# Kernel tuning notes

Hardware: AMD Instinct MI355X
Metric: run time of the kernel (lower is better)

The kernel has to match this reference:

```python
import jax, jax.numpy as jnp
import numpy as np

N_NODES = 100000
N_EDGES = 1600000  # avg degree 16
D_FEAT = 128


def setup_inputs() -> dict:
    key = jax.random.key(0)
    k1, k2, k3 = jax.random.split(key, 3)
    x = jax.random.normal(k1, (N_NODES, D_FEAT), dtype=jnp.float32)
    edge_index = jax.random.randint(k2, (2, N_EDGES), 0, N_NODES, dtype=jnp.int64)
    edge_values = jax.random.uniform(k3, (N_EDGES,), dtype=jnp.float32)
    return {"x": x, "edge_index": edge_index, "edge_values": edge_values}


def reference(x, edge_index, edge_values):
    # torch_sparse.spmm(indices, values, N, N, x):
    # out[row_e] += values[e] * x[col_e]  for each COO edge e.
    row, col = edge_index[0], edge_index[1]
    msgs = edge_values[:, None] * x[col]              # [E, D] gathered messages
    out = jax.ops.segment_sum(msgs, row, num_segments=x.shape[0])  # [N, D]
    return out
```

## Files before the change

### kernel.cpp

```cpp
#include <hip/hip_runtime.h>
#include <hip/hip_bf16.h>


#define D_FEAT 128
#define CAP 32
#define CAP_S 40
#define OVF_CAP 8192
#define CONV_BLOCKS 1024
#define EPB 2048
#define BIN_SHIFT 9
#define SEG_CAP 9216

typedef float f32x4 __attribute__((ext_vector_type(4)));

static __device__ __forceinline__ unsigned short f2bf(float f) {
    unsigned u = __float_as_uint(f);
    u += 0x7fffu + ((u >> 16) & 1u);
    return (unsigned short)(u >> 16);
}


__global__ __launch_bounds__(256) void conv_part_kernel(
    const float* __restrict__ x, unsigned* __restrict__ xq32,
    float* __restrict__ scales, int N,
    const int* __restrict__ rows, const int* __restrict__ cols,
    const float* __restrict__ w,
    int* __restrict__ binfill,
    unsigned long long* __restrict__ part,
    unsigned long long* __restrict__ ovf,
    int E) {
    __shared__ unsigned long long ldsbuf[EPB];
    __shared__ int hist[256];
    __shared__ int tmp[256];
    __shared__ int boff[256];
    __shared__ int base_s[256];

    int tid = threadIdx.x;

    if (blockIdx.x < CONV_BLOCKS) {
        int grp = tid >> 5;
        int gl  = tid & 31;
        const float4* x4 = reinterpret_cast<const float4*>(x);
        for (int r = blockIdx.x * 8 + grp; r < N; r += CONV_BLOCKS * 8) {
            float4 v = x4[(size_t)r * 32 + gl];
            float m = fmaxf(fmaxf(fabsf(v.x), fabsf(v.y)),
                            fmaxf(fabsf(v.z), fabsf(v.w)));
            m = fmaxf(m, __shfl_xor(m, 1));
            m = fmaxf(m, __shfl_xor(m, 2));
            m = fmaxf(m, __shfl_xor(m, 4));
            m = fmaxf(m, __shfl_xor(m, 8));
            m = fmaxf(m, __shfl_xor(m, 16));
            float rs = (m > 0.f) ? 127.0f / m : 0.f;
            int q0 = __float2int_rn(v.x * rs) + 128;
            int q1 = __float2int_rn(v.y * rs) + 128;
            int q2 = __float2int_rn(v.z * rs) + 128;
            int q3 = __float2int_rn(v.w * rs) + 128;
            q0 = min(max(q0, 0), 255); q1 = min(max(q1, 0), 255);
            q2 = min(max(q2, 0), 255); q3 = min(max(q3, 0), 255);
            unsigned pk = (unsigned)q0 | ((unsigned)q1 << 8)
                        | ((unsigned)q2 << 16) | ((unsigned)q3 << 24);
            __builtin_nontemporal_store(pk, &xq32[(size_t)r * 32 + gl]);
            if (gl == 0) scales[r] = m * (1.0f / 127.0f);
        }
        return;
    }

    int pb = blockIdx.x - CONV_BLOCKS;
    int ebase = pb * EPB;

    hist[tid] = 0;
    __syncthreads();

    unsigned long long e64[8];
    unsigned meta[8];
#pragma unroll 8
    for (int j = 0; j < 8; ++j) {
        int idx = ebase + tid + j * 256;
        if (idx < E) {
            int r = rows[idx];
            int c = cols[idx];
            float wv = w[idx];
            int bin = r >> BIN_SHIFT;
            int rk = atomicAdd(&hist[bin], 1);
            e64[j] = (unsigned long long)(unsigned)r
                   | ((unsigned long long)(unsigned)c << 17)
                   | ((unsigned long long)f2bf(wv) << 34);
            meta[j] = ((unsigned)bin << 13) | (unsigned)rk;
        } else {
            meta[j] = 0xffffffffu;
        }
    }
    __syncthreads();

    int hv = hist[tid];
    tmp[tid] = hv;
    __syncthreads();
    for (int off = 1; off < 256; off <<= 1) {
        int t = (tid >= off) ? tmp[tid - off] : 0;
        __syncthreads();
        tmp[tid] += t;
        __syncthreads();
    }
    boff[tid] = tmp[tid] - hv;
    int total = tmp[255];

    base_s[tid] = atomicAdd(&binfill[tid], hv);
#pragma unroll 8
    for (int j = 0; j < 8; ++j) {
        if (meta[j] != 0xffffffffu) {
            int bin = meta[j] >> 13;
            int rk = meta[j] & 0x1fff;
            ldsbuf[boff[bin] + rk] = e64[j];
        }
    }
    __syncthreads();

    int* ovfcnt = binfill + 256;
    for (int k = tid; k < total; k += 256) {
        unsigned long long e = ldsbuf[k];
        int bin = (int)(e & 0x1ffffu) >> BIN_SHIFT;
        int pos = base_s[bin] + (k - boff[bin]);
        if (pos < SEG_CAP) {
            part[(size_t)bin * SEG_CAP + pos] = e;
        } else {
            int o = atomicAdd(ovfcnt, 1);
            if (o < OVF_CAP) ovf[o] = e;
        }
    }
}


__global__ __launch_bounds__(512) void bucketize_kernel(
    const unsigned long long* __restrict__ part, int* __restrict__ binfill,
    const float* __restrict__ scales,
    unsigned* __restrict__ packed, int* __restrict__ cursor,
    unsigned long long* __restrict__ ovf, int N) {
    __shared__ int cnt[512];
    int b = blockIdx.x;
    int tid = threadIdx.x;
    cnt[tid] = 0;
    __syncthreads();

    int fill = min(binfill[b], SEG_CAP);
    int rbase = b << BIN_SHIFT;
    const unsigned long long* seg = part + (size_t)b * SEG_CAP;
    int* ovfcnt = binfill + 256;

    for (int k = tid; k < fill; k += 512) {
        unsigned long long e = seg[k];
        int r = (int)(e & 0x1ffffu);
        int rk = atomicAdd(&cnt[r - rbase], 1);
        if (rk < CAP) {
            unsigned c = (unsigned)(e >> 17) & 0x1ffffu;
            float wv = __uint_as_float((unsigned)((e >> 34) & 0xffffu) << 16);
            float wf = wv * scales[c];
            packed[(size_t)r * CAP_S + rk] = c | ((unsigned)f2bf(wf) << 17);
        } else {
            int o = atomicAdd(ovfcnt, 1);
            if (o < OVF_CAP) ovf[o] = e;
        }
    }
    __syncthreads();

    int r = rbase + tid;
    if (r < N) {
        int d = min(cnt[tid], CAP);
        int pad = min((d + 7) & ~7, CAP);
        unsigned* pb = packed + (size_t)r * CAP_S;
        for (int k = d; k < pad; ++k) pb[k] = 0u;
        cursor[r] = pad;
    }
}


__global__ __launch_bounds__(256) void spmm_cap_kernel(
    const unsigned* __restrict__ xq32,
    const int* __restrict__ cursor, const unsigned* __restrict__ packed,
    float* __restrict__ out, int N) {
    int wid = (int)((blockIdx.x * 256 + threadIdx.x) >> 6);
    int lane = threadIdx.x & 63;
    int gl = lane & 31;
    bool hi = lane >= 32;
    if (wid >= N) return;

    int deg = cursor[wid];
    float a0 = 0.f, a1 = 0.f, a2 = 0.f, a3 = 0.f, sumw = 0.f;

    if (deg > 0) {
        const unsigned* base = packed + (size_t)wid * CAP_S;
        const unsigned* xl = xq32 + gl;
        uint4 pa = *reinterpret_cast<const uint4*>(base);
        uint4 pb = *reinterpret_cast<const uint4*>(base + 4);
        for (int e = 0; e < deg; e += 8) {
            const unsigned* nb = base + e + 8;
            uint4 qa = *reinterpret_cast<const uint4*>(nb);
            uint4 qb = *reinterpret_cast<const uint4*>(nb + 4);
            unsigned e0 = hi ? pa.y : pa.x;
            unsigned e1 = hi ? pa.w : pa.z;
            unsigned e2 = hi ? pb.y : pb.x;
            unsigned e3 = hi ? pb.w : pb.z;
            unsigned u0 = xl[(e0 & 0x1ffffu) << 5];
            unsigned u1 = xl[(e1 & 0x1ffffu) << 5];
            unsigned u2 = xl[(e2 & 0x1ffffu) << 5];
            unsigned u3 = xl[(e3 & 0x1ffffu) << 5];
            float w0 = __uint_as_float((e0 >> 17) << 16);
            float w1 = __uint_as_float((e1 >> 17) << 16);
            float w2 = __uint_as_float((e2 >> 17) << 16);
            float w3 = __uint_as_float((e3 >> 17) << 16);
            a0 += w0 * (float)(u0 & 0xffu);
            a1 += w0 * (float)((u0 >> 8) & 0xffu);
            a2 += w0 * (float)((u0 >> 16) & 0xffu);
            a3 += w0 * (float)(u0 >> 24);
            a0 += w1 * (float)(u1 & 0xffu);
            a1 += w1 * (float)((u1 >> 8) & 0xffu);
            a2 += w1 * (float)((u1 >> 16) & 0xffu);
            a3 += w1 * (float)(u1 >> 24);
            a0 += w2 * (float)(u2 & 0xffu);
            a1 += w2 * (float)((u2 >> 8) & 0xffu);
            a2 += w2 * (float)((u2 >> 16) & 0xffu);
            a3 += w2 * (float)(u2 >> 24);
            a0 += w3 * (float)(u3 & 0xffu);
            a1 += w3 * (float)((u3 >> 8) & 0xffu);
            a2 += w3 * (float)((u3 >> 16) & 0xffu);
            a3 += w3 * (float)(u3 >> 24);
            sumw += w0 + w1 + w2 + w3;
            pa = qa; pb = qb;
        }
    }
    a0 -= 128.0f * sumw; a1 -= 128.0f * sumw;
    a2 -= 128.0f * sumw; a3 -= 128.0f * sumw;
    a0 += __shfl_xor(a0, 32);
    a1 += __shfl_xor(a1, 32);
    a2 += __shfl_xor(a2, 32);
    a3 += __shfl_xor(a3, 32);
    if (!hi) {
        f32x4 o; o.x = a0; o.y = a1; o.z = a2; o.w = a3;
        __builtin_nontemporal_store(
            o, reinterpret_cast<f32x4*>(out) + (size_t)wid * 32 + gl);
    }
}


__global__ __launch_bounds__(256) void cleanup_kernel(
    const float* __restrict__ x, const unsigned long long* __restrict__ ovf,
    const int* __restrict__ binfill, float* __restrict__ out) {
    int t = blockIdx.x * 256 + threadIdx.x;
    int i = t >> 5;
    int part_ = t & 31;
    int cnt = min(binfill[256], OVF_CAP);
    if (i >= cnt) return;
    unsigned long long e = ovf[i];
    int r = (int)(e & 0x1ffffu);
    int c = (int)((e >> 17) & 0x1ffffu);
    float wv = __uint_as_float((unsigned)((e >> 34) & 0xffffu) << 16);
    const float4* xr = reinterpret_cast<const float4*>(x + (size_t)c * D_FEAT);
    float4 v = xr[part_];
    float* o = out + (size_t)r * D_FEAT + part_ * 4;
    unsafeAtomicAdd(o + 0, v.x * wv);
    unsafeAtomicAdd(o + 1, v.y * wv);
    unsafeAtomicAdd(o + 2, v.z * wv);
    unsafeAtomicAdd(o + 3, v.w * wv);
}


__global__ __launch_bounds__(256) void spmm_scatter_kernel(
    const float* __restrict__ x, const int* __restrict__ edge_index,
    const float* __restrict__ edge_values, float* __restrict__ out, int E) {
    long long t = (long long)blockIdx.x * blockDim.x + threadIdx.x;
    int e = (int)(t >> 5);
    int part = (int)(t & 31);
    if (e >= E) return;
    int row = edge_index[e];
    int col = edge_index[E + e];
    float w = edge_values[e];
    const float4* xrow = reinterpret_cast<const float4*>(x + (size_t)col * D_FEAT);
    float4 v = xrow[part];
    float* o = out + (size_t)row * D_FEAT + part * 4;
    unsafeAtomicAdd(o + 0, v.x * w);
    unsafeAtomicAdd(o + 1, v.y * w);
    unsafeAtomicAdd(o + 2, v.z * w);
    unsafeAtomicAdd(o + 3, v.w * w);
}


extern "C" void kernel_launch(void* const* d_in, const int* in_sizes, int n_in,
                              void* d_out, int out_size, void* d_ws, size_t ws_size,
                              hipStream_t stream) {
    const float* x           = (const float*)d_in[0];
    const int*   edge_index  = (const int*)d_in[1];
    const float* edge_values = (const float*)d_in[2];
    float*       out         = (float*)d_out;

    int E = in_sizes[2];
    int N = out_size / D_FEAT;
    const int* rows = edge_index;
    const int* cols = edge_index + E;
    int nbins = (N + (1 << BIN_SHIFT) - 1) >> BIN_SHIFT;

    size_t off = 0;
    int* cursor  = (int*)((char*)d_ws + off); off += (size_t)N * sizeof(int);
    int* binfill = (int*)((char*)d_ws + off); off += 257 * sizeof(int);
    off = (off + 127) & ~(size_t)127;
    float* scales = (float*)((char*)d_ws + off); off += (size_t)N * sizeof(float);
    off = (off + 127) & ~(size_t)127;
    unsigned long long* ovf = (unsigned long long*)((char*)d_ws + off);
    off += (size_t)OVF_CAP * sizeof(unsigned long long);
    unsigned long long* part = (unsigned long long*)((char*)d_ws + off);
    off += (size_t)nbins * SEG_CAP * sizeof(unsigned long long);
    off = (off + 127) & ~(size_t)127;
    unsigned* packed = (unsigned*)((char*)d_ws + off);
    off += (size_t)N * CAP_S * sizeof(unsigned);
    off = (off + 127) & ~(size_t)127;
    unsigned* xq32 = (unsigned*)((char*)d_ws + off);
    off += (size_t)N * 32 * sizeof(unsigned);

    if (off <= ws_size && N <= (1 << 17) && nbins <= 256) {
        int pbl = (E + EPB - 1) / EPB;
        int gbl = (int)(((long long)N * 64 + 255) / 256);
        hipMemsetAsync(binfill, 0, 257 * sizeof(int), stream);
        conv_part_kernel<<<CONV_BLOCKS + pbl, 256, 0, stream>>>(
            x, xq32, scales, N, rows, cols, edge_values, binfill, part, ovf, E);
        bucketize_kernel<<<nbins, 512, 0, stream>>>(
            part, binfill, scales, packed, cursor, ovf, N);
        spmm_cap_kernel<<<gbl, 256, 0, stream>>>(
            xq32, cursor, packed, out, N);
        cleanup_kernel<<<(OVF_CAP * 32) / 256, 256, 0, stream>>>(
            x, ovf, binfill, out);
        return;
    }

    hipMemsetAsync(d_out, 0, (size_t)out_size * sizeof(float), stream);
    long long total_threads = (long long)E * 32;
    long long grid = (total_threads + 255) / 256;
    spmm_scatter_kernel<<<(dim3)(unsigned)grid, 256, 0, stream>>>(
        x, edge_index, edge_values, out, E);
}
```

Before: 107.4 us.

## Process two rows per wavefront in spmm and use wave-shuffle scan for bins

The spmm kernel now assigns two output rows to each 64-lane wavefront and interleaves their gathers, which halves the wave count and doubles the memory-level parallelism per wave. Each row's weight sum is reduced across the wave once before it is subtracted. The block prefix scan in the partition kernel is replaced with a shuffle-based wave scan plus a small cross-wave add, removing many __syncthreads. Padding now zeroes each row to CAP so the shared loop bound max(degA,degB) reads zeros for the shorter row, which costs extra stores and wasted iterations when the two degrees differ.

```diff
diff --git a/kernel.cpp b/kernel.cpp
--- a/kernel.cpp
+++ b/kernel.cpp
@@ -31,9 +31,9 @@
     int E) {
     __shared__ unsigned long long ldsbuf[EPB];
     __shared__ int hist[256];
-    __shared__ int tmp[256];
     __shared__ int boff[256];
     __shared__ int base_s[256];
+    __shared__ int wsum[4];
 
     int tid = threadIdx.x;
 
@@ -93,16 +93,21 @@
     __syncthreads();
 
     int hv = hist[tid];
-    tmp[tid] = hv;
-    __syncthreads();
-    for (int off = 1; off < 256; off <<= 1) {
-        int t = (tid >= off) ? tmp[tid - off] : 0;
-        __syncthreads();
-        tmp[tid] += t;
-        __syncthreads();
-    }
-    boff[tid] = tmp[tid] - hv;
-    int total = tmp[255];
+    int s = hv;
+#pragma unroll
+    for (int d = 1; d < 64; d <<= 1) {
+        int t = __shfl_up(s, d);
+        if ((tid & 63) >= d) s += t;
+    }
+    if ((tid & 63) == 63) wsum[tid >> 6] = s;
+    __syncthreads();
+    int wv_ = tid >> 6;
+    int add = 0;
+#pragma unroll
+    for (int k = 0; k < 4; ++k) add += (k < wv_) ? wsum[k] : 0;
+    boff[tid] = s - hv + add;
+    int total = wsum[0] + wsum[1] + wsum[2] + wsum[3];
+    __syncthreads();
 
     base_s[tid] = atomicAdd(&binfill[tid], hv);
 #pragma unroll 8
@@ -165,9 +170,9 @@
     int r = rbase + tid;
     if (r < N) {
         int d = min(cnt[tid], CAP);
-        int pad = min((d + 7) & ~7, CAP);
+        int pad = (d + 7) & ~7;
         unsigned* pb = packed + (size_t)r * CAP_S;
-        for (int k = d; k < pad; ++k) pb[k] = 0u;
+        for (int k = d; k < CAP; ++k) pb[k] = 0u;
         cursor[r] = pad;
     }
 }
@@ -177,66 +182,116 @@
     const unsigned* __restrict__ xq32,
     const int* __restrict__ cursor, const unsigned* __restrict__ packed,
     float* __restrict__ out, int N) {
-    int wid = (int)((blockIdx.x * 256 + threadIdx.x) >> 6);
+    int gw = (int)((blockIdx.x * 256 + threadIdx.x) >> 6);
+    int rA = gw * 2;
+    if (rA >= N) return;
+    int rB = rA + 1;
+    bool hasB = rB < N;
     int lane = threadIdx.x & 63;
     int gl = lane & 31;
     bool hi = lane >= 32;
-    if (wid >= N) return;
-
-    int deg = cursor[wid];
-    float a0 = 0.f, a1 = 0.f, a2 = 0.f, a3 = 0.f, sumw = 0.f;
+
+    int degA = cursor[rA];
+    int degB = hasB ? cursor[rB] : 0;
+    int deg = max(degA, degB);
+
+    float a0 = 0.f, a1 = 0.f, a2 = 0.f, a3 = 0.f, swA = 0.f;
+    float b0 = 0.f, b1 = 0.f, b2 = 0.f, b3 = 0.f, swB = 0.f;
 
     if (deg > 0) {
-        const unsigned* base = packed + (size_t)wid * CAP_S;
+        const unsigned* baseA = packed + (size_t)rA * CAP_S;
+        const unsigned* baseB = packed + (size_t)(hasB ? rB : rA) * CAP_S;
         const unsigned* xl = xq32 + gl;
-        uint4 pa = *reinterpret_cast<const uint4*>(base);
-        uint4 pb = *reinterpret_cast<const uint4*>(base + 4);
+        uint4 paA = *reinterpret_cast<const uint4*>(baseA);
+        uint4 pbA = *reinterpret_cast<const uint4*>(baseA + 4);
+        uint4 paB = *reinterpret_cast<const uint4*>(baseB);
+        uint4 pbB = *reinterpret_cast<const uint4*>(baseB + 4);
         for (int e = 0; e < deg; e += 8) {
-            const unsigned* nb = base + e + 8;
-            uint4 qa = *reinterpret_cast<const uint4*>(nb);
-            uint4 qb = *reinterpret_cast<const uint4*>(nb + 4);
-            unsigned e0 = hi ? pa.y : pa.x;
-            unsigned e1 = hi ? pa.w : pa.z;
-            unsigned e2 = hi ? pb.y : pb.x;
-            unsigned e3 = hi ? pb.w : pb.z;
-            unsigned u0 = xl[(e0 & 0x1ffffu) << 5];
-            unsigned u1 = xl[(e1 & 0x1ffffu) << 5];
-            unsigned u2 = xl[(e2 & 0x1ffffu) << 5];
-            unsigned u3 = xl[(e3 & 0x1ffffu) << 5];
-            float w0 = __uint_as_float((e0 >> 17) << 16);
-            float w1 = __uint_as_float((e1 >> 17) << 16);
-            float w2 = __uint_as_float((e2 >> 17) << 16);
-            float w3 = __uint_as_float((e3 >> 17) << 16);
-            a0 += w0 * (float)(u0 & 0xffu);
-            a1 += w0 * (float)((u0 >> 8) & 0xffu);
-            a2 += w0 * (float)((u0 >> 16) & 0xffu);
-            a3 += w0 * (float)(u0 >> 24);
-            a0 += w1 * (float)(u1 & 0xffu);
-            a1 += w1 * (float)((u1 >> 8) & 0xffu);
-            a2 += w1 * (float)((u1 >> 16) & 0xffu);
-            a3 += w1 * (float)(u1 >> 24);
-            a0 += w2 * (float)(u2 & 0xffu);
-            a1 += w2 * (float)((u2 >> 8) & 0xffu);
-            a2 += w2 * (float)((u2 >> 16) & 0xffu);
-            a3 += w2 * (float)(u2 >> 24);
-            a0 += w3 * (float)(u3 & 0xffu);
-            a1 += w3 * (float)((u3 >> 8) & 0xffu);
-            a2 += w3 * (float)((u3 >> 16) & 0xffu);
-            a3 += w3 * (float)(u3 >> 24);
-            sumw += w0 + w1 + w2 + w3;
-            pa = qa; pb = qb;
-        }
-    }
-    a0 -= 128.0f * sumw; a1 -= 128.0f * sumw;
-    a2 -= 128.0f * sumw; a3 -= 128.0f * sumw;
-    a0 += __shfl_xor(a0, 32);
-    a1 += __shfl_xor(a1, 32);
-    a2 += __shfl_xor(a2, 32);
-    a3 += __shfl_xor(a3, 32);
+            const unsigned* nA = baseA + e + 8;
+            const unsigned* nB = baseB + e + 8;
+            uint4 qaA = *reinterpret_cast<const uint4*>(nA);
+            uint4 qbA = *reinterpret_cast<const uint4*>(nA + 4);
+            uint4 qaB = *reinterpret_cast<const uint4*>(nB);
+            uint4 qbB = *reinterpret_cast<const uint4*>(nB + 4);
+            unsigned eA0 = hi ? paA.y : paA.x;
+            unsigned eA1 = hi ? paA.w : paA.z;
+            unsigned eA2 = hi ? pbA.y : pbA.x;
+            unsigned eA3 = hi ? pbA.w : pbA.z;
+            unsigned eB0 = hi ? paB.y : paB.x;
+            unsigned eB1 = hi ? paB.w : paB.z;
+            unsigned eB2 = hi ? pbB.y : pbB.x;
+            unsigned eB3 = hi ? pbB.w : pbB.z;
+            unsigned uA0 = xl[(eA0 & 0x1ffffu) << 5];
+            unsigned uA1 = xl[(eA1 & 0x1ffffu) << 5];
+            unsigned uA2 = xl[(eA2 & 0x1ffffu) << 5];
+            unsigned uA3 = xl[(eA3 & 0x1ffffu) << 5];
+            unsigned uB0 = xl[(eB0 & 0x1ffffu) << 5];
+            unsigned uB1 = xl[(eB1 & 0x1ffffu) << 5];
+            unsigned uB2 = xl[(eB2 & 0x1ffffu) << 5];
+            unsigned uB3 = xl[(eB3 & 0x1ffffu) << 5];
+            float wA0 = __uint_as_float((eA0 >> 17) << 16);
+            float wA1 = __uint_as_float((eA1 >> 17) << 16);
+            float wA2 = __uint_as_float((eA2 >> 17) << 16);
+            float wA3 = __uint_as_float((eA3 >> 17) << 16);
+            float wB0 = __uint_as_float((eB0 >> 17) << 16);
+            float wB1 = __uint_as_float((eB1 >> 17) << 16);
+            float wB2 = __uint_as_float((eB2 >> 17) << 16);
+            float wB3 = __uint_as_float((eB3 >> 17) << 16);
+            a0 += wA0 * (float)(uA0 & 0xffu);
+            a1 += wA0 * (float)((uA0 >> 8) & 0xffu);
+            a2 += wA0 * (float)((uA0 >> 16) & 0xffu);
+            a3 += wA0 * (float)(uA0 >> 24);
+            a0 += wA1 * (float)(uA1 & 0xffu);
+            a1 += wA1 * (float)((uA1 >> 8) & 0xffu);
+            a2 += wA1 * (float)((uA1 >> 16) & 0xffu);
+            a3 += wA1 * (float)(uA1 >> 24);
+            a0 += wA2 * (float)(uA2 & 0xffu);
+            a1 += wA2 * (float)((uA2 >> 8) & 0xffu);
+            a2 += wA2 * (float)((uA2 >> 16) & 0xffu);
+            a3 += wA2 * (float)(uA2 >> 24);
+            a0 += wA3 * (float)(uA3 & 0xffu);
+            a1 += wA3 * (float)((uA3 >> 8) & 0xffu);
+            a2 += wA3 * (float)((uA3 >> 16) & 0xffu);
+            a3 += wA3 * (float)(uA3 >> 24);
+            b0 += wB0 * (float)(uB0 & 0xffu);
+            b1 += wB0 * (float)((uB0 >> 8) & 0xffu);
+            b2 += wB0 * (float)((uB0 >> 16) & 0xffu);
+            b3 += wB0 * (float)(uB0 >> 24);
+            b0 += wB1 * (float)(uB1 & 0xffu);
+            b1 += wB1 * (float)((uB1 >> 8) & 0xffu);
+            b2 += wB1 * (float)((uB1 >> 16) & 0xffu);
+            b3 += wB1 * (float)(uB1 >> 24);
+            b0 += wB2 * (float)(uB2 & 0xffu);
+            b1 += wB2 * (float)((uB2 >> 8) & 0xffu);
+            b2 += wB2 * (float)((uB2 >> 16) & 0xffu);
+            b3 += wB2 * (float)(uB2 >> 24);
+            b0 += wB3 * (float)(uB3 & 0xffu);
+            b1 += wB3 * (float)((uB3 >> 8) & 0xffu);
+            b2 += wB3 * (float)((uB3 >> 16) & 0xffu);
+            b3 += wB3 * (float)(uB3 >> 24);
+            swA += wA0 + wA1 + wA2 + wA3;
+            swB += wB0 + wB1 + wB2 + wB3;
+            paA = qaA; pbA = qbA; paB = qaB; pbB = qbB;
+        }
+    }
+    a0 += __shfl_xor(a0, 32); a1 += __shfl_xor(a1, 32);
+    a2 += __shfl_xor(a2, 32); a3 += __shfl_xor(a3, 32);
+    swA += __shfl_xor(swA, 32);
+    b0 += __shfl_xor(b0, 32); b1 += __shfl_xor(b1, 32);
+    b2 += __shfl_xor(b2, 32); b3 += __shfl_xor(b3, 32);
+    swB += __shfl_xor(swB, 32);
     if (!hi) {
-        f32x4 o; o.x = a0; o.y = a1; o.z = a2; o.w = a3;
+        f32x4 o;
+        o.x = a0 - 128.0f * swA; o.y = a1 - 128.0f * swA;
+        o.z = a2 - 128.0f * swA; o.w = a3 - 128.0f * swA;
         __builtin_nontemporal_store(
-            o, reinterpret_cast<f32x4*>(out) + (size_t)wid * 32 + gl);
+            o, reinterpret_cast<f32x4*>(out) + (size_t)rA * 32 + gl);
+    } else if (hasB) {
+        f32x4 o;
+        o.x = b0 - 128.0f * swB; o.y = b1 - 128.0f * swB;
+        o.z = b2 - 128.0f * swB; o.w = b3 - 128.0f * swB;
+        __builtin_nontemporal_store(
+            o, reinterpret_cast<f32x4*>(out) + (size_t)rB * 32 + gl);
     }
 }
 
@@ -316,7 +371,8 @@
 
     if (off <= ws_size && N <= (1 << 17) && nbins <= 256) {
         int pbl = (E + EPB - 1) / EPB;
-        int gbl = (int)(((long long)N * 64 + 255) / 256);
+        int waves = (N + 1) / 2;
+        int gbl = (waves + 3) / 4;
         hipMemsetAsync(binfill, 0, 257 * sizeof(int), stream);
         conv_part_kernel<<<CONV_BLOCKS + pbl, 256, 0, stream>>>(
             x, xq32, scales, N, rows, cols, edge_values, binfill, part, ovf, E);
```

After: 103.1 us. 4.0% less time.
